# Optimization experiments

Measured on AMD Instinct MI355X. Metric: run time of the kernel, lower is better.

Reference implementation:

```python
import jax, jax.numpy as jnp
import numpy as np

DIM = 1024
DIM_INNER = 1536  # int(1024 * 1.5)


def _log_g(x):
    # log of g(x) = where(x>=0, x+0.5, sigmoid(x)) computed stably in log-space
    return jnp.where(x >= 0.0, jnp.log(jnp.maximum(x, 0.0) + 0.5), -jax.nn.softplus(-x))


def _heinsen_scan_log(log_coefficients, log_values):
    # parallel associative scan in log space over the sequence axis (axis=1)
    a_star = jnp.cumsum(log_coefficients, axis=1)
    log_h0_plus_b_star = jax.lax.cumlogsumexp(log_values - a_star, axis=1)
    return jnp.exp(a_star + log_h0_plus_b_star)


def _forward_gru(x, W_hg, W_out):
    # x: [b, s, dim] -> hidden/gate: [b, s, dim_inner]
    hg = jnp.einsum('bsd,ed->bse', x, W_hg)
    hidden, gate = jnp.split(hg, 2, axis=-1)
    log_coefficients = -jax.nn.softplus(gate)      # log(1 - z)
    log_z = -jax.nn.softplus(-gate)                # log z
    log_values = log_z + _log_g(hidden)
    out = _heinsen_scan_log(log_coefficients, log_values)  # [b, s, dim_inner]
    return jnp.einsum('bse,de->bsd', out, W_out)


def setup_inputs() -> dict:
    key = jax.random.key(0)
    k1, k2, k3 = jax.random.split(key, 3)
    x = jax.random.normal(k1, (4, 4096, DIM), dtype=jnp.float32)
    W_hg = jax.random.normal(k2, (2 * DIM_INNER, DIM), dtype=jnp.float32) * (DIM ** -0.5)
    W_out = jax.random.normal(k3, (DIM, DIM_INNER), dtype=jnp.float32) * (DIM_INNER ** -0.5)
    return {"x": x, "W_hg": W_hg, "W_out": W_out}


def reference(x, W_hg, W_out):
    out_forward = _forward_gru(x, W_hg, W_out)
    # bidirectional=True: run on time-flipped input and add (module does NOT flip back)
    out_backward = _forward_gru(jnp.flip(x, axis=1), W_hg, W_out)
    return out_forward + out_backward
```

## Files before the change

kernel.cpp:

```cpp
#include <hip/hip_runtime.h>
#include <hip/hip_fp16.h>
#include <cstdint>
#include <cstddef>

#define B_ 4
#define S_ 4096
#define D_ 1024
#define E_ 1536
#define M_ (B_*S_)
#define BE_ (B_*E_)
#define C_ 32
#define L_ (S_/C_)

typedef short bf16x8 __attribute__((ext_vector_type(8)));
typedef float f32x4 __attribute__((ext_vector_type(4)));

__device__ __forceinline__ unsigned short f2b(float f) {
  union { float f; unsigned int i; } x; x.f = f;
  unsigned int r = x.i + 0x7FFFu + ((x.i >> 16) & 1u);
  return (unsigned short)(r >> 16);
}
__device__ __forceinline__ float h2f(unsigned short u) { return __half2float(__ushort_as_half(u)); }
__device__ __forceinline__ unsigned int packcv(float c, float v) {
  return (unsigned int)__half_as_ushort(__float2half_rn(c)) |
         ((unsigned int)__half_as_ushort(__float2half_rn(v)) << 16);
}

__global__ __launch_bounds__(256) void cvt_bf16(const float* __restrict__ src,
                                                unsigned short* __restrict__ dst) {
  const int i = blockIdx.x * 256 + threadIdx.x;
  float4 f = ((const float4*)src)[i];
  ushort4 u; u.x = f2b(f.x); u.y = f2b(f.y); u.z = f2b(f.z); u.w = f2b(f.w);
  ((ushort4*)dst)[i] = u;
}

__global__ __launch_bounds__(256) void gemm1_mfma(const unsigned short* __restrict__ Xb,
                                                  const unsigned short* __restrict__ Wb,
                                                  unsigned int* __restrict__ CV) {
  __shared__ unsigned short lA[128 * 32];
  __shared__ unsigned short lB[128 * 32];
  const int t = threadIdx.x;
  const int m0 = blockIdx.x * 128;
  const int n0 = blockIdx.y * 64;
  const int wv = t >> 6, lane = t & 63;
  const int wm = wv >> 1, we = wv & 1;
  const int lm = lane & 15, kg = lane >> 4;
  const int r1 = t >> 2, q1 = t & 3;
  const int r2 = r1 + 64;
  const int gb1 = (r1 < 64) ? (n0 + r1) : (E_ + n0 + r1 - 64);
  const int gb2 = (r2 < 64) ? (n0 + r2) : (E_ + n0 + r2 - 64);

  const f32x4 z4 = {0.f, 0.f, 0.f, 0.f};
  f32x4 ah[4][2], ag[4][2];
#pragma unroll
  for (int i = 0; i < 4; ++i)
#pragma unroll
    for (int j = 0; j < 2; ++j) { ah[i][j] = z4; ag[i][j] = z4; }

  for (int k0 = 0; k0 < D_; k0 += 32) {
    *(uint4*)(lA + (size_t)r1 * 32 + q1 * 8) = *(const uint4*)(Xb + (size_t)(m0 + r1) * D_ + k0 + q1 * 8);
    *(uint4*)(lA + (size_t)r2 * 32 + q1 * 8) = *(const uint4*)(Xb + (size_t)(m0 + r2) * D_ + k0 + q1 * 8);
    *(uint4*)(lB + (size_t)r1 * 32 + q1 * 8) = *(const uint4*)(Wb + (size_t)gb1 * D_ + k0 + q1 * 8);
    *(uint4*)(lB + (size_t)r2 * 32 + q1 * 8) = *(const uint4*)(Wb + (size_t)gb2 * D_ + k0 + q1 * 8);
    __syncthreads();
    bf16x8 af[4], bh[2], bg[2];
#pragma unroll
    for (int mt = 0; mt < 4; ++mt)
      af[mt] = *(const bf16x8*)(lA + (size_t)(wm * 64 + mt * 16 + lm) * 32 + kg * 8);
#pragma unroll
    for (int et = 0; et < 2; ++et) {
      bh[et] = *(const bf16x8*)(lB + (size_t)(we * 32 + et * 16 + lm) * 32 + kg * 8);
      bg[et] = *(const bf16x8*)(lB + (size_t)(64 + we * 32 + et * 16 + lm) * 32 + kg * 8);
    }
#pragma unroll
    for (int mt = 0; mt < 4; ++mt)
#pragma unroll
      for (int et = 0; et < 2; ++et) {
        ah[mt][et] = __builtin_amdgcn_mfma_f32_16x16x32_bf16(af[mt], bh[et], ah[mt][et], 0, 0, 0);
        ag[mt][et] = __builtin_amdgcn_mfma_f32_16x16x32_bf16(af[mt], bg[et], ag[mt][et], 0, 0, 0);
      }
    __syncthreads();
  }
#pragma unroll
  for (int mt = 0; mt < 4; ++mt)
#pragma unroll
    for (int et = 0; et < 2; ++et) {
      const int e = n0 + we * 32 + et * 16 + lm;
#pragma unroll
      for (int r = 0; r < 4; ++r) {
        const int m = m0 + wm * 64 + mt * 16 + kg * 4 + r;
        const float hid = ah[mt][et][r];
        const float gat = ag[mt][et][r];
        const float z = 1.f / (1.f + expf(-gat));
        const float c = 1.f / (1.f + expf(gat));
        const float gv = (hid >= 0.f) ? (hid + 0.5f) : (1.f / (1.f + expf(-hid)));
        CV[(size_t)m * E_ + e] = packcv(c, z * gv);
      }
    }
}

__global__ __launch_bounds__(256) void scan_p1(const unsigned int* __restrict__ CV,
                                               float* __restrict__ P, float* __restrict__ Qf,
                                               float* __restrict__ Qr) {
  const int be = blockIdx.x * 256 + threadIdx.x;
  const int b = be / E_, e = be - b * E_;
  const int k = blockIdx.y;
  const unsigned int* cv = CV + (size_t)b * S_ * E_ + e + (size_t)k * L_ * E_;
  float pp = 1.f, qf = 0.f, qr = 0.f;
  for (int l = 0; l < L_; ++l) {
    const unsigned int p = cv[(size_t)l * E_];
    const float c = h2f((unsigned short)p), v = h2f((unsigned short)(p >> 16));
    qf = fmaf(c, qf, v);
    qr = fmaf(pp, v, qr);
    pp *= c;
  }
  P[(size_t)k * BE_ + be] = pp;
  Qf[(size_t)k * BE_ + be] = qf;
  Qr[(size_t)k * BE_ + be] = qr;
}

__global__ __launch_bounds__(256) void scan_p2(const float* __restrict__ P, const float* __restrict__ Qf,
                                               const float* __restrict__ Qr, float* __restrict__ HfIn,
                                               float* __restrict__ HbIn) {
  const int be = blockIdx.x * 256 + threadIdx.x;
  float hf = 0.f;
  for (int k = 0; k < C_; ++k) {
    HfIn[(size_t)k * BE_ + be] = hf;
    hf = fmaf(P[(size_t)k * BE_ + be], hf, Qf[(size_t)k * BE_ + be]);
  }
  float hb = 0.f;
  for (int k = C_ - 1; k >= 0; --k) {
    HbIn[(size_t)k * BE_ + be] = hb;
    hb = fmaf(P[(size_t)k * BE_ + be], hb, Qr[(size_t)k * BE_ + be]);
  }
}

__global__ __launch_bounds__(256) void scan_p3(const unsigned int* __restrict__ CV,
                                               const float* __restrict__ HfIn,
                                               const float* __restrict__ HbIn,
                                               unsigned short* __restrict__ Hb) {
  const int be = blockIdx.x * 256 + threadIdx.x;
  const int b = be / E_, e = be - b * E_;
  const int k = blockIdx.y;
  const unsigned int* cv = CV + (size_t)b * S_ * E_ + e;
  const unsigned int* cvf = cv + (size_t)k * L_ * E_;
  const unsigned int* cvb = cv + (size_t)(S_ - 1 - k * L_) * E_;
  unsigned short* hp = Hb + (size_t)b * S_ * E_ + e + (size_t)k * L_ * E_;
  float hf = HfIn[(size_t)k * BE_ + be];
  float hb = HbIn[(size_t)(C_ - 1 - k) * BE_ + be];
  for (int l = 0; l < L_; ++l) {
    const unsigned int pf = cvf[(size_t)l * E_];
    const unsigned int pb = *(cvb - (ptrdiff_t)l * E_);
    hf = fmaf(h2f((unsigned short)pf), hf, h2f((unsigned short)(pf >> 16)));
    hb = fmaf(h2f((unsigned short)pb), hb, h2f((unsigned short)(pb >> 16)));
    hp[(size_t)l * E_] = f2b(hf + hb);
  }
}

__global__ __launch_bounds__(256) void gemm2_mfma(const unsigned short* __restrict__ Hb,
                                                  const unsigned short* __restrict__ Wob,
                                                  float* __restrict__ Out) {
  __shared__ unsigned short lA[128 * 32];
  __shared__ unsigned short lB[128 * 32];
  const int t = threadIdx.x;
  const int m0 = blockIdx.x * 128;
  const int n0 = blockIdx.y * 128;
  const int wv = t >> 6, lane = t & 63;
  const int wm = wv >> 1, wn = wv & 1;
  const int lm = lane & 15, kg = lane >> 4;
  const int r1 = t >> 2, q1 = t & 3;
  const int r2 = r1 + 64;

  const f32x4 z4 = {0.f, 0.f, 0.f, 0.f};
  f32x4 acc[4][4];
#pragma unroll
  for (int i = 0; i < 4; ++i)
#pragma unroll
    for (int j = 0; j < 4; ++j) acc[i][j] = z4;

  for (int k0 = 0; k0 < E_; k0 += 32) {
    *(uint4*)(lA + (size_t)r1 * 32 + q1 * 8) = *(const uint4*)(Hb + (size_t)(m0 + r1) * E_ + k0 + q1 * 8);
    *(uint4*)(lA + (size_t)r2 * 32 + q1 * 8) = *(const uint4*)(Hb + (size_t)(m0 + r2) * E_ + k0 + q1 * 8);
    *(uint4*)(lB + (size_t)r1 * 32 + q1 * 8) = *(const uint4*)(Wob + (size_t)(n0 + r1) * E_ + k0 + q1 * 8);
    *(uint4*)(lB + (size_t)r2 * 32 + q1 * 8) = *(const uint4*)(Wob + (size_t)(n0 + r2) * E_ + k0 + q1 * 8);
    __syncthreads();
    bf16x8 af[4], bf[4];
#pragma unroll
    for (int mt = 0; mt < 4; ++mt)
      af[mt] = *(const bf16x8*)(lA + (size_t)(wm * 64 + mt * 16 + lm) * 32 + kg * 8);
#pragma unroll
    for (int nt = 0; nt < 4; ++nt)
      bf[nt] = *(const bf16x8*)(lB + (size_t)(wn * 64 + nt * 16 + lm) * 32 + kg * 8);
#pragma unroll
    for (int mt = 0; mt < 4; ++mt)
#pragma unroll
      for (int nt = 0; nt < 4; ++nt)
        acc[mt][nt] = __builtin_amdgcn_mfma_f32_16x16x32_bf16(af[mt], bf[nt], acc[mt][nt], 0, 0, 0);
    __syncthreads();
  }
#pragma unroll
  for (int mt = 0; mt < 4; ++mt)
#pragma unroll
    for (int nt = 0; nt < 4; ++nt) {
      const int d = n0 + wn * 64 + nt * 16 + lm;
#pragma unroll
      for (int r = 0; r < 4; ++r) {
        const int m = m0 + wm * 64 + mt * 16 + kg * 4 + r;
        Out[(size_t)m * D_ + d] = acc[mt][nt][r];
      }
    }
}

extern "C" void kernel_launch(void* const* d_in, const int* in_sizes, int n_in,
                              void* d_out, int out_size, void* d_ws, size_t ws_size,
                              hipStream_t stream) {
  const float* x    = (const float*)d_in[0];
  const float* whg  = (const float*)d_in[1];
  const float* wout = (const float*)d_in[2];
  float* out = (float*)d_out;

  unsigned int*  CV = (unsigned int*)d_ws;
  unsigned short* Hb = (unsigned short*)((char*)d_ws + (size_t)M_ * E_ * 4);
  unsigned short* Xb  = Hb;
  unsigned short* Wb  = Xb + (size_t)M_ * D_;
  unsigned short* Wob = (unsigned short*)d_ws;
  float* P    = out;
  float* Qf   = out + (size_t)C_ * BE_;
  float* Qr   = out + 2 * (size_t)C_ * BE_;
  float* HfIn = out + 3 * (size_t)C_ * BE_;
  float* HbIn = out + 4 * (size_t)C_ * BE_;

  cvt_bf16<<<M_ * D_ / 1024, 256, 0, stream>>>(x, Xb);
  cvt_bf16<<<2 * E_ * D_ / 1024, 256, 0, stream>>>(whg, Wb);
  gemm1_mfma<<<dim3(M_ / 128, E_ / 64), 256, 0, stream>>>(Xb, Wb, CV);
  scan_p1<<<dim3(BE_ / 256, C_), 256, 0, stream>>>(CV, P, Qf, Qr);
  scan_p2<<<BE_ / 256, 256, 0, stream>>>(P, Qf, Qr, HfIn, HbIn);
  scan_p3<<<dim3(BE_ / 256, C_), 256, 0, stream>>>(CV, HfIn, HbIn, Hb);
  cvt_bf16<<<D_ * E_ / 1024, 256, 0, stream>>>(wout, Wob);
  gemm2_mfma<<<dim3(M_ / 128, D_ / 128), 256, 0, stream>>>(Hb, Wob, out);
}
```

Before: 416.9 us.

## Use direct global-to-LDS loads in GEMMs, fuse conversions, cheaper sigmoid, unroll scans

Both GEMMs now stage tiles through global_load_lds async copies instead of register round-trips. GEMM1 moves to a K-step of 64 with a wave-specialized staging layout. The two bf16 conversion launches are merged into one kernel, and the epilogue uses __expf with c = 1 - z instead of a second exponential. The scan loops get unroll pragmas to expose more loads in flight. Risks are LDS bank conflicts from the new layout and small accuracy changes from the fast exp.

```diff
diff --git a/kernel.cpp b/kernel.cpp
--- a/kernel.cpp
+++ b/kernel.cpp
@@ -25,6 +25,10 @@
   return (unsigned int)__half_as_ushort(__float2half_rn(c)) |
          ((unsigned int)__half_as_ushort(__float2half_rn(v)) << 16);
 }
+__device__ __forceinline__ void async16(const unsigned short* g, unsigned short* l) {
+  __builtin_amdgcn_global_load_lds((const __attribute__((address_space(1))) unsigned int*)g,
+                                   (__attribute__((address_space(3))) unsigned int*)l, 16, 0, 0);
+}
 
 __global__ __launch_bounds__(256) void cvt_bf16(const float* __restrict__ src,
                                                 unsigned short* __restrict__ dst) {
@@ -34,21 +38,42 @@
   ((ushort4*)dst)[i] = u;
 }
 
+#define NB_X   (M_*D_/1024)
+#define NB_WHG (2*E_*D_/1024)
+__global__ __launch_bounds__(256) void cvt_xw(const float* __restrict__ x, unsigned short* __restrict__ xb,
+                                              const float* __restrict__ whg, unsigned short* __restrict__ wb) {
+  int blk = blockIdx.x;
+  const float* src; unsigned short* dst;
+  if (blk < NB_X) { src = x; dst = xb; }
+  else            { blk -= NB_X; src = whg; dst = wb; }
+  const int i = blk * 256 + threadIdx.x;
+  float4 f = ((const float4*)src)[i];
+  ushort4 u; u.x = f2b(f.x); u.y = f2b(f.y); u.z = f2b(f.z); u.w = f2b(f.w);
+  ((ushort4*)dst)[i] = u;
+}
+
 __global__ __launch_bounds__(256) void gemm1_mfma(const unsigned short* __restrict__ Xb,
                                                   const unsigned short* __restrict__ Wb,
                                                   unsigned int* __restrict__ CV) {
-  __shared__ unsigned short lA[128 * 32];
-  __shared__ unsigned short lB[128 * 32];
+  __shared__ unsigned short lA[128 * 64];
+  __shared__ unsigned short lB[128 * 64];
   const int t = threadIdx.x;
   const int m0 = blockIdx.x * 128;
   const int n0 = blockIdx.y * 64;
   const int wv = t >> 6, lane = t & 63;
   const int wm = wv >> 1, we = wv & 1;
   const int lm = lane & 15, kg = lane >> 4;
-  const int r1 = t >> 2, q1 = t & 3;
-  const int r2 = r1 + 64;
-  const int gb1 = (r1 < 64) ? (n0 + r1) : (E_ + n0 + r1 - 64);
-  const int gb2 = (r2 < 64) ? (n0 + r2) : (E_ + n0 + r2 - 64);
+  const int srow = lane >> 3, scol = lane & 7;
+  const bool stageA = (wv < 2);
+  const unsigned short* gbase;
+  if (stageA) {
+    gbase = Xb + (size_t)(m0 + (wv * 64) + srow) * D_ + scol * 8;
+  } else {
+    const int rloc = (wv - 2) * 64 + srow;
+    const int gr = (rloc < 64) ? (n0 + rloc) : (E_ + n0 + rloc - 64);
+    gbase = Wb + (size_t)gr * D_ + scol * 8;
+  }
+  unsigned short* lbase = (stageA ? lA : lB) + (size_t)(wv & 1) * 4096;
 
   const f32x4 z4 = {0.f, 0.f, 0.f, 0.f};
   f32x4 ah[4][2], ag[4][2];
@@ -57,28 +82,30 @@
 #pragma unroll
     for (int j = 0; j < 2; ++j) { ah[i][j] = z4; ag[i][j] = z4; }
 
-  for (int k0 = 0; k0 < D_; k0 += 32) {
-    *(uint4*)(lA + (size_t)r1 * 32 + q1 * 8) = *(const uint4*)(Xb + (size_t)(m0 + r1) * D_ + k0 + q1 * 8);
-    *(uint4*)(lA + (size_t)r2 * 32 + q1 * 8) = *(const uint4*)(Xb + (size_t)(m0 + r2) * D_ + k0 + q1 * 8);
-    *(uint4*)(lB + (size_t)r1 * 32 + q1 * 8) = *(const uint4*)(Wb + (size_t)gb1 * D_ + k0 + q1 * 8);
-    *(uint4*)(lB + (size_t)r2 * 32 + q1 * 8) = *(const uint4*)(Wb + (size_t)gb2 * D_ + k0 + q1 * 8);
-    __syncthreads();
-    bf16x8 af[4], bh[2], bg[2];
-#pragma unroll
-    for (int mt = 0; mt < 4; ++mt)
-      af[mt] = *(const bf16x8*)(lA + (size_t)(wm * 64 + mt * 16 + lm) * 32 + kg * 8);
-#pragma unroll
-    for (int et = 0; et < 2; ++et) {
-      bh[et] = *(const bf16x8*)(lB + (size_t)(we * 32 + et * 16 + lm) * 32 + kg * 8);
-      bg[et] = *(const bf16x8*)(lB + (size_t)(64 + we * 32 + et * 16 + lm) * 32 + kg * 8);
-    }
-#pragma unroll
-    for (int mt = 0; mt < 4; ++mt)
+  for (int k0 = 0; k0 < D_; k0 += 64) {
+#pragma unroll
+    for (int j = 0; j < 8; ++j)
+      async16(gbase + k0 + (size_t)(j * 8) * D_, lbase + (size_t)j * 512);
+    __syncthreads();
+#pragma unroll
+    for (int kh = 0; kh < 2; ++kh) {
+      bf16x8 af[4], bh[2], bg[2];
+#pragma unroll
+      for (int mt = 0; mt < 4; ++mt)
+        af[mt] = *(const bf16x8*)(lA + (size_t)(wm * 64 + mt * 16 + lm) * 64 + kh * 32 + kg * 8);
 #pragma unroll
       for (int et = 0; et < 2; ++et) {
-        ah[mt][et] = __builtin_amdgcn_mfma_f32_16x16x32_bf16(af[mt], bh[et], ah[mt][et], 0, 0, 0);
-        ag[mt][et] = __builtin_amdgcn_mfma_f32_16x16x32_bf16(af[mt], bg[et], ag[mt][et], 0, 0, 0);
-      }
+        bh[et] = *(const bf16x8*)(lB + (size_t)(we * 32 + et * 16 + lm) * 64 + kh * 32 + kg * 8);
+        bg[et] = *(const bf16x8*)(lB + (size_t)(64 + we * 32 + et * 16 + lm) * 64 + kh * 32 + kg * 8);
+      }
+#pragma unroll
+      for (int mt = 0; mt < 4; ++mt)
+#pragma unroll
+        for (int et = 0; et < 2; ++et) {
+          ah[mt][et] = __builtin_amdgcn_mfma_f32_16x16x32_bf16(af[mt], bh[et], ah[mt][et], 0, 0, 0);
+          ag[mt][et] = __builtin_amdgcn_mfma_f32_16x16x32_bf16(af[mt], bg[et], ag[mt][et], 0, 0, 0);
+        }
+    }
     __syncthreads();
   }
 #pragma unroll
@@ -91,9 +118,9 @@
         const int m = m0 + wm * 64 + mt * 16 + kg * 4 + r;
         const float hid = ah[mt][et][r];
         const float gat = ag[mt][et][r];
-        const float z = 1.f / (1.f + expf(-gat));
-        const float c = 1.f / (1.f + expf(gat));
-        const float gv = (hid >= 0.f) ? (hid + 0.5f) : (1.f / (1.f + expf(-hid)));
+        const float z = 1.f / (1.f + __expf(-gat));
+        const float c = 1.f - z;
+        const float gv = (hid >= 0.f) ? (hid + 0.5f) : (1.f / (1.f + __expf(-hid)));
         CV[(size_t)m * E_ + e] = packcv(c, z * gv);
       }
     }
@@ -105,8 +132,9 @@
   const int be = blockIdx.x * 256 + threadIdx.x;
   const int b = be / E_, e = be - b * E_;
   const int k = blockIdx.y;
-  const unsigned int* cv = CV + (size_t)b * S_ * E_ + e + (size_t)k * L_ * E_;
+  const unsigned int* cv = CV + ((size_t)b * S_ + (size_t)k * L_) * E_ + e;
   float pp = 1.f, qf = 0.f, qr = 0.f;
+#pragma unroll 8
   for (int l = 0; l < L_; ++l) {
     const unsigned int p = cv[(size_t)l * E_];
     const float c = h2f((unsigned short)p), v = h2f((unsigned short)(p >> 16));
@@ -142,12 +170,12 @@
   const int be = blockIdx.x * 256 + threadIdx.x;
   const int b = be / E_, e = be - b * E_;
   const int k = blockIdx.y;
-  const unsigned int* cv = CV + (size_t)b * S_ * E_ + e;
-  const unsigned int* cvf = cv + (size_t)k * L_ * E_;
-  const unsigned int* cvb = cv + (size_t)(S_ - 1 - k * L_) * E_;
-  unsigned short* hp = Hb + (size_t)b * S_ * E_ + e + (size_t)k * L_ * E_;
+  const unsigned int* cvf = CV + ((size_t)b * S_ + (size_t)k * L_) * E_ + e;
+  const unsigned int* cvb = CV + ((size_t)b * S_ + (size_t)(S_ - 1 - k * L_)) * E_ + e;
+  unsigned short* hp = Hb + ((size_t)b * S_ + (size_t)k * L_) * E_ + e;
   float hf = HfIn[(size_t)k * BE_ + be];
   float hb = HbIn[(size_t)(C_ - 1 - k) * BE_ + be];
+#pragma unroll 8
   for (int l = 0; l < L_; ++l) {
     const unsigned int pf = cvf[(size_t)l * E_];
     const unsigned int pb = *(cvb - (ptrdiff_t)l * E_);
@@ -168,8 +196,7 @@
   const int wv = t >> 6, lane = t & 63;
   const int wm = wv >> 1, wn = wv & 1;
   const int lm = lane & 15, kg = lane >> 4;
-  const int r1 = t >> 2, q1 = t & 3;
-  const int r2 = r1 + 64;
+  const int lrow = lane >> 2, lq = lane & 3;
 
   const f32x4 z4 = {0.f, 0.f, 0.f, 0.f};
   f32x4 acc[4][4];
@@ -179,10 +206,17 @@
     for (int j = 0; j < 4; ++j) acc[i][j] = z4;
 
   for (int k0 = 0; k0 < E_; k0 += 32) {
-    *(uint4*)(lA + (size_t)r1 * 32 + q1 * 8) = *(const uint4*)(Hb + (size_t)(m0 + r1) * E_ + k0 + q1 * 8);
-    *(uint4*)(lA + (size_t)r2 * 32 + q1 * 8) = *(const uint4*)(Hb + (size_t)(m0 + r2) * E_ + k0 + q1 * 8);
-    *(uint4*)(lB + (size_t)r1 * 32 + q1 * 8) = *(const uint4*)(Wob + (size_t)(n0 + r1) * E_ + k0 + q1 * 8);
-    *(uint4*)(lB + (size_t)r2 * 32 + q1 * 8) = *(const uint4*)(Wob + (size_t)(n0 + r2) * E_ + k0 + q1 * 8);
+#pragma unroll
+    for (int j = 0; j < 4; ++j) {
+      const int c = (wv << 2) | j;
+      if (c < 8) {
+        const int row = c * 16 + lrow;
+        async16(Hb + (size_t)(m0 + row) * E_ + k0 + lq * 8, lA + (size_t)c * 512);
+      } else {
+        const int row = (c - 8) * 16 + lrow;
+        async16(Wob + (size_t)(n0 + row) * E_ + k0 + lq * 8, lB + (size_t)(c - 8) * 512);
+      }
+    }
     __syncthreads();
     bf16x8 af[4], bf[4];
 #pragma unroll
@@ -230,8 +264,7 @@
   float* HfIn = out + 3 * (size_t)C_ * BE_;
   float* HbIn = out + 4 * (size_t)C_ * BE_;
 
-  cvt_bf16<<<M_ * D_ / 1024, 256, 0, stream>>>(x, Xb);
-  cvt_bf16<<<2 * E_ * D_ / 1024, 256, 0, stream>>>(whg, Wb);
+  cvt_xw<<<NB_X + NB_WHG, 256, 0, stream>>>(x, Xb, whg, Wb);
   gemm1_mfma<<<dim3(M_ / 128, E_ / 64), 256, 0, stream>>>(Xb, Wb, CV);
   scan_p1<<<dim3(BE_ / 256, C_), 256, 0, stream>>>(CV, P, Qf, Qr);
   scan_p2<<<BE_ / 256, 256, 0, stream>>>(P, Qf, Qr, HfIn, HbIn);
```

Measured after the change: 400.2 us. 1.04x faster.
